# Kernel optimization log

Measured on AMD Instinct MI355X. Metric: run time of the kernel, lower is better.

Reference implementation:

```python
import jax, jax.numpy as jnp
from jax import lax
import numpy as np

B, IMG_H, IMG_W = 8, 256, 512
NUM_CLASSES, P = 20, 32
SCALE, TOPK, IOU_THR = 32.0, 100, 0.5


def conv2d(x, w, b, stride=1, pad=1):
    y = lax.conv_general_dilated(x, w, (stride, stride), [(pad, pad), (pad, pad)],
                                 dimension_numbers=('NCHW', 'OIHW', 'NCHW'))
    return y + b[None, :, None, None]


def bilinear_resize(img, out_h, out_w):
    # img: [..., H, W]; torch F.interpolate(mode='bilinear', align_corners=False)
    H, W = img.shape[-2], img.shape[-1]
    def idx_w(n_in, n_out):
        src = (jnp.arange(n_out, dtype=jnp.float32) + 0.5) * (n_in / n_out) - 0.5
        src = jnp.clip(src, 0.0, n_in - 1)
        i0 = jnp.floor(src).astype(jnp.int32)
        i1 = jnp.minimum(i0 + 1, n_in - 1)
        return i0, i1, src - i0.astype(jnp.float32)
    y0, y1, wy = idx_w(H, out_h)
    x0, x1, wx = idx_w(W, out_w)
    top = img[..., y0, :] * (1.0 - wy)[:, None] + img[..., y1, :] * wy[:, None]
    return top[..., x0] * (1.0 - wx) + top[..., x1] * wx


def generate_anchors(fh, fw):
    ys = (jnp.arange(fh, dtype=jnp.float32) + 0.5) * (IMG_H / fh)
    xs = (jnp.arange(fw, dtype=jnp.float32) + 0.5) * (IMG_W / fw)
    cy, cx = jnp.meshgrid(ys, xs, indexing='ij')
    h = SCALE / 2
    return jnp.stack([cx - h, cy - h, cx + h, cy + h], -1).reshape(-1, 4)


def delta_to_boxes(anchors, deltas):
    a_c = (anchors[:, :2] + anchors[:, 2:]) / 2
    a_wh = anchors[:, 2:] - anchors[:, :2]
    pc = a_c + deltas[..., :2] * a_wh
    pwh = a_wh * jnp.exp(deltas[..., 2:])
    return jnp.concatenate([pc - pwh / 2, pc + pwh / 2], -1)


def nms_single(boxes, scores, labels):
    # torchvision batched_nms: offset boxes per label, greedy NMS, return kept idxs
    N = boxes.shape[0]
    off = labels.astype(boxes.dtype) * (jnp.max(boxes) + 1.0)
    b = boxes + off[:, None]
    order = jnp.argsort(-scores)
    bs = b[order]
    area = (bs[:, 2] - bs[:, 0]) * (bs[:, 3] - bs[:, 1])
    lt = jnp.maximum(bs[:, None, :2], bs[None, :, :2])
    rb = jnp.minimum(bs[:, None, 2:], bs[None, :, 2:])
    wh = jnp.clip(rb - lt, 0.0)
    inter = wh[..., 0] * wh[..., 1]
    iou = inter / (area[:, None] + area[None, :] - inter + 1e-9)
    idxs = jnp.arange(N)
    def body(i, suppressed):
        keep_i = jnp.logical_not(suppressed[i])
        row = (iou[i] > IOU_THR) & (idxs > i)
        return jnp.where(keep_i, suppressed | row, suppressed)
    suppressed = lax.fori_loop(0, N, body, jnp.zeros(N, bool))
    keep_mask = ~suppressed
    rank = jnp.cumsum(keep_mask) - 1
    slots = jnp.where(keep_mask & (rank < TOPK), rank, TOPK)
    out = jnp.full(TOPK + 1, -1, jnp.int32).at[slots].set(order.astype(jnp.int32))
    return out[:TOPK]


def setup_inputs():
    key = jax.random.key(0)
    ks = jax.random.split(key, 17)
    def cw(k, o, i, kh, kw_):
        return jax.random.normal(k, (o, i, kh, kw_), jnp.float32) / np.sqrt(i * kh * kw_)
    return {
        'images': jax.random.normal(ks[0], (B, 3, IMG_H, IMG_W), jnp.float32),
        'w1': cw(ks[1], 64, 3, 3, 3),   'b1': jnp.zeros(64, jnp.float32),
        'w2': cw(ks[2], 128, 64, 3, 3), 'b2': jnp.zeros(128, jnp.float32),
        'w3': cw(ks[3], 256, 128, 3, 3),'b3': jnp.zeros(256, jnp.float32),
        'pw1': cw(ks[4], 256, 256, 3, 3), 'pb1': jnp.zeros(256, jnp.float32),
        'pw2': cw(ks[5], P, 256, 1, 1),   'pb2': jnp.zeros(P, jnp.float32),
        'cw_': cw(ks[6], NUM_CLASSES + 1, 256, 3, 3), 'cb': jnp.zeros(NUM_CLASSES + 1, jnp.float32),
        'bw': cw(ks[7], 4, 256, 3, 3),  'bb': jnp.zeros(4, jnp.float32),
        'kw': cw(ks[8], P, 256, 3, 3),  'kb': jnp.zeros(P, jnp.float32),
    }


def reference(images, w1, b1, w2, b2, w3, b3, pw1, pb1, pw2, pb2, cw_, cb, bw, bb, kw, kb):
    x = jax.nn.relu(conv2d(images, w1, b1, stride=2))
    x = jax.nn.relu(conv2d(x, w2, b2, stride=2))
    feat = jax.nn.relu(conv2d(x, w3, b3, stride=2))          # [B,256,32,64]
    proto = conv2d(jax.nn.relu(conv2d(feat, pw1, pb1)), pw2, pb2, pad=0)  # [B,P,32,64]
    fh, fw = feat.shape[2], feat.shape[3]
    def head(w, b, c):
        return conv2d(feat, w, b).transpose(0, 2, 3, 1).reshape(B, -1, c)
    cls = head(cw_, cb, NUM_CLASSES + 1)     # [B,N,C+1]
    box = head(bw, bb, 4)                    # [B,N,4]
    coef = head(kw, kb, P)                   # [B,N,P]
    anchors = generate_anchors(fh, fw)       # [N,4]
    probs = jax.nn.softmax(cls, -1)[..., :-1]
    scores = probs.max(-1)
    labels = probs.argmax(-1).astype(jnp.int32)
    boxes = delta_to_boxes(anchors, box)     # [B,N,4]
    keep = jax.vmap(nms_single)(boxes, scores, labels)   # [B,100], -1 pad
    valid = keep >= 0
    ki = jnp.clip(keep, 0)
    take = lambda a: jnp.take_along_axis(a, ki[..., None] if a.ndim == 3 else ki, axis=1)
    boxes_k = take(boxes) * valid[..., None]
    scores_k = take(scores) * valid
    labels_k = jnp.where(valid, take(labels), 0)
    coef_k = jnp.take_along_axis(coef, ki[..., None], axis=1)   # [B,100,P]
    m = jax.nn.sigmoid(jnp.einsum('bkp,bphw->bkhw', coef_k, proto))
    masks = bilinear_resize(m, IMG_H, IMG_W) > 0.5
    masks = masks & valid[..., None, None]
    return boxes_k, scores_k, labels_k, masks, valid
```

## Files before the change

kernel.cpp:

```cpp
#include <hip/hip_runtime.h>
#include <hip/hip_bf16.h>
#include <math.h>

#define BB 8
#define NCLS 21
#define NANCH 2048
#define TOPK_N 100

static const size_t OFF_X1HI = 0;
static const size_t OFF_X1LO = 34344960;
static const size_t OFF_X2HI = 68689920;
static const size_t OFF_X2LO = 86261760;
static const size_t OFF_FTHI = 103833600;
static const size_t OFF_FTLO = 113025024;
static const size_t OFF_WT1  = 122216448;
static const size_t OFF_A2H  = 122223616;
static const size_t OFF_A2L  = 122371072;
static const size_t OFF_A3H  = 122518528;
static const size_t OFF_A3L  = 123108352;
static const size_t OFF_AHH  = 123698176;
static const size_t OFF_AHL  = 123993088;
static const size_t OFF_AP1H = 124288000;
static const size_t OFF_AP1L = 125467648;
static const size_t OFF_WTP2 = 126647296;
static const size_t OFF_BH   = 126680064;
static const size_t OFF_HOUT = 126680576;
static const size_t OFF_P1   = 130874880;
static const size_t OFF_PROTO= 147652096;
static const size_t OFF_BOXES= 149749248;
static const size_t OFF_SCORES=150011392;
static const size_t OFF_LABELS=150076928;
static const size_t OFF_ORDER= 150142464;
static const size_t OFF_SB   = 150208000;
static const size_t OFF_IOU  = 150470144;
static const size_t OFF_KEEP = 154664448;
static const size_t OFF_MAXB = 154668032;

static const size_t OUT_BOXES  = 0;
static const size_t OUT_SCORES = 3200;
static const size_t OUT_LABELS = 4000;
static const size_t OUT_MASKS  = 4800;
static const size_t OUT_VALID  = 104862400;

typedef __attribute__((ext_vector_type(8))) short bf16x8;
typedef __attribute__((ext_vector_type(4))) float f32x4;

__device__ __forceinline__ unsigned encf(float f){
  unsigned u = __float_as_uint(f);
  return (u & 0x80000000u) ? ~u : (u | 0x80000000u);
}
__device__ __forceinline__ float decf(unsigned u){
  unsigned b = (u & 0x80000000u) ? (u & 0x7fffffffu) : ~u;
  return __uint_as_float(b);
}
__device__ __forceinline__ short f2bf(float f){
  __hip_bfloat16 h = __float2bfloat16(f);
  return *(short*)&h;
}
__device__ __forceinline__ float bf2f(short h){
  return __uint_as_float(((unsigned)(unsigned short)h) << 16);
}

template<int CIN,int COUT,int KK>
__device__ __forceinline__ void packw_body(int i, const float* __restrict__ w,
                                           float* __restrict__ wT){
  if (i >= CIN*KK*COUT) return;
  int co = i % COUT; int r = i / COUT;
  int ci = r / KK,  k = r % KK;
  wT[i] = w[(co*CIN + ci)*KK + k];
}

template<int CIN,int COUT>
__device__ __forceinline__ void packA_body(int i, const float* __restrict__ w,
                                           short* __restrict__ Ahi, short* __restrict__ Alo){
  constexpr int K = CIN*9;
  constexpr int KS = K/32;
  if (i >= COUT*K) return;
  int sub  = i & 7;
  int lane = (i >> 3) & 63;
  int rest = i >> 9;
  int ks = rest % KS;
  int mt = rest / KS;
  int m = mt*16 + (lane & 15);
  int k = ks*32 + (lane >> 4)*8 + sub;
  int tap = k / CIN, ci = k - tap*CIN;
  float v = w[(m*CIN + ci)*9 + tap];
  short h = f2bf(v);
  Ahi[i] = h;
  Alo[i] = f2bf(v - bf2f(h));
}

__device__ __forceinline__ void packAh_body(int i,
    const float* __restrict__ cw, const float* __restrict__ bw,
    const float* __restrict__ kw, const float* __restrict__ cb,
    const float* __restrict__ bb, const float* __restrict__ kb,
    short* __restrict__ Ahi, short* __restrict__ Alo, float* __restrict__ bh){
  if (i < 64){
    float v = 0.f;
    if (i < 21) v = cb[i]; else if (i < 25) v = bb[i-21]; else if (i < 57) v = kb[i-25];
    bh[i] = v;
  }
  if (i >= 64*2304) return;
  constexpr int KS = 72;
  int sub  = i & 7;
  int lane = (i >> 3) & 63;
  int rest = i >> 9;
  int ks = rest % KS;
  int mt = rest / KS;
  int m = mt*16 + (lane & 15);
  int k = ks*32 + (lane >> 4)*8 + sub;
  int tap = k >> 8, ci = k & 255;
  float v = 0.f;
  if (m < 21)      v = cw[(m*256 + ci)*9 + tap];
  else if (m < 25) v = bw[((m-21)*256 + ci)*9 + tap];
  else if (m < 57) v = kw[((m-25)*256 + ci)*9 + tap];
  short h = f2bf(v);
  Ahi[i] = h;
  Alo[i] = f2bf(v - bf2f(h));
}

__global__ __launch_bounds__(256) void megaprep(
    const float* __restrict__ images, const float* __restrict__ w1, const float* __restrict__ b1,
    const float* __restrict__ w2, short* __restrict__ a2h, short* __restrict__ a2l,
    const float* __restrict__ w3, short* __restrict__ a3h, short* __restrict__ a3l,
    const float* __restrict__ pw1, short* __restrict__ ap1h, short* __restrict__ ap1l,
    const float* __restrict__ cw, const float* __restrict__ bw, const float* __restrict__ kw,
    const float* __restrict__ cb, const float* __restrict__ bb, const float* __restrict__ kb,
    short* __restrict__ ahh, short* __restrict__ ahl, float* __restrict__ bh,
    const float* __restrict__ pw2, float* __restrict__ wTp2,
    short* __restrict__ x1hi, short* __restrict__ x1lo,
    short* __restrict__ x2hi, short* __restrict__ x2lo,
    short* __restrict__ fthi, short* __restrict__ ftlo,
    unsigned* __restrict__ maxb){
  __shared__ float sw[27*64];
  const int blk = blockIdx.x, tid = threadIdx.x;

  if (blk < 583){
    int i = blk*256 + tid;
    if (i < BB) maxb[i] = 0u;
    short *hi, *lo; int Hp, Wp, cell, bg;
    if (i < 49408){
      hi=x1hi; lo=x1lo; Hp=130; Wp=258; cell = i % 772; bg = i / 772;
    } else if (i < 99072){
      int j = i - 49408; hi=x2hi; lo=x2lo; Hp=66; Wp=130; cell = j % 388; bg = j / 388;
    } else if (i < 149248){
      int j = i - 99072; hi=fthi; lo=ftlo; Hp=34; Wp=66; cell = j % 196; bg = j / 196;
    } else return;
    int y, x;
    if (cell < Wp)        { y = 0;      x = cell; }
    else if (cell < 2*Wp) { y = Hp-1;   x = cell - Wp; }
    else { int r = cell - 2*Wp; y = 1 + (r>>1); x = (r&1) ? (Wp-1) : 0; }
    size_t ad = (((size_t)bg*Hp + y)*Wp + x)*8;
    bf16x8 z = (bf16x8){0,0,0,0,0,0,0,0};
    *(bf16x8*)(hi + ad) = z;
    *(bf16x8*)(lo + ad) = z;
    return;
  }
  if (blk < 4935){
    int lb = blk - 583;
    if (lb < 288)        packA_body<64,128>(lb*256+tid, w2, a2h, a2l);
    else if (lb < 1440)  packA_body<128,256>((lb-288)*256+tid, w3, a3h, a3l);
    else if (lb < 3744)  packA_body<256,256>((lb-1440)*256+tid, pw1, ap1h, ap1l);
    else if (lb < 4320)  packAh_body((lb-3744)*256+tid, cw,bw,kw,cb,bb,kb, ahh,ahl,bh);
    else                 packw_body<256,32,1>((lb-4320)*256+tid, pw2, wTp2);
    return;
  }

  const int cblk = blk - 4935;
  const int bxc = cblk & 63;
  const int co0 = ((cblk >> 6) & 3) * 16;
  const int b   = cblk >> 8;
  for (int idx = tid; idx < 1728; idx += 256){
    int r = idx >> 6, co = idx & 63;
    sw[idx] = w1[co*27 + r];
  }
  __syncthreads();

  const int g  = bxc*256 + tid;
  const int y  = g >> 7;
  const int x0 = (g & 127) << 1;

  float acc[16][2];
#pragma unroll
  for (int c=0;c<16;c++){
    float bv = b1[co0+c];
    acc[c][0] = bv; acc[c][1] = bv;
  }
  int   off[3][5];
  float msk[3][5];
#pragma unroll
  for (int kh=0;kh<3;kh++){
    int iy = y*2 - 1 + kh;
    bool okr = (iy >= 0) && (iy < 256);
    int ro = okr ? iy*512 : 0;
#pragma unroll
    for (int t=0;t<5;t++){
      int col = x0*2 - 1 + t;
      bool ok = okr && (col >= 0) && (col < 512);
      off[kh][t] = ok ? (ro + col) : 0;
      msk[kh][t] = ok ? 1.f : 0.f;
    }
  }
  const float* inb = images + (size_t)b*3*256*512;
  for (int ci=0; ci<3; ci++){
    const float* inc = inb + (size_t)ci*256*512;
    float v[3][5];
#pragma unroll
    for (int kh=0;kh<3;kh++)
#pragma unroll
      for (int t=0;t<5;t++)
        v[kh][t] = inc[off[kh][t]] * msk[kh][t];
    const float* wp = sw + ci*9*64 + co0;
#pragma unroll
    for (int kh=0;kh<3;kh++)
#pragma unroll
    for (int kw2=0;kw2<3;kw2++){
      const float* wq = wp + (kh*3+kw2)*64;
#pragma unroll
      for (int c=0;c<16;c++){
        float wv = wq[c];
        acc[c][0] = fmaf(wv, v[kh][2*0+kw2], acc[c][0]);
        acc[c][1] = fmaf(wv, v[kh][2*1+kw2], acc[c][1]);
      }
    }
  }
#pragma unroll
  for (int s=0;s<2;s++){
    short hv[16] __attribute__((aligned(16)));
    short lv[16] __attribute__((aligned(16)));
#pragma unroll
    for (int c=0;c<16;c++){
      float r = fmaxf(acc[c][s], 0.f);
      short h = f2bf(r);
      hv[c] = h;
      lv[c] = f2bf(r - bf2f(h));
    }
#pragma unroll
    for (int g2=0; g2<2; g2++){
      size_t ad = (((size_t)(b*8 + (co0>>3) + g2)*130 + (y+1))*258 + (x0+s+1))*8;
      *(bf16x8*)(x1hi + ad) = *(bf16x8*)(hv + g2*8);
      *(bf16x8*)(x1lo + ad) = *(bf16x8*)(lv + g2*8);
    }
  }
}

template<int CIN,int K,int M,int MW,int NW,int S,int IPH,int IPW,int NXB,
         bool SPLIT,bool STAGELO,bool STAGEREG,int EMODE,int OPH,int OPW>
__device__ __forceinline__ void cgemm_row_body(
    short* sB, int bxi, int byi, int bzi,
    const short* __restrict__ Ahi, const short* __restrict__ Alo,
    const short* __restrict__ Bhi, const short* __restrict__ Blo,
    const float* __restrict__ bias, float* __restrict__ outf,
    short* __restrict__ outhi, short* __restrict__ outlo){
  static_assert(CIN % 32 == 0, "CIN must be multiple of 32");
  constexpr int NT = 64*32;
  constexpr int KS = K/32;
  constexpr int CG = CIN/8;
  constexpr int SW  = 64*S + 2;
  constexpr int SWP = (S==2) ? (SW/2 + 1) : SW;
  constexpr int LOOFF = CG*((S==2)?2:1)*SWP*8;
  constexpr int NTH = NW*64;
  constexpr int NLD = (CG*SW + NTH - 1)/NTH;

  const int b    = bzi;
  const int oy   = bxi / NXB;
  const int xb   = (bxi % NXB) * 64;
  const int wave = threadIdx.x >> 6;
  const int lane = threadIdx.x & 63;
  const int lm = lane & 15, lq = lane >> 4;
  const int m0 = (byi * NW + wave) * (MW*16);
  const int tid = threadIdx.x;

  f32x4 acc[MW][4];
#pragma unroll
  for (int i=0;i<MW;i++)
#pragma unroll
    for (int j=0;j<4;j++) acc[i][j] = (f32x4){0.f,0.f,0.f,0.f};

  const short* Ah_l = Ahi + (size_t)lane*8;
  const short* Al_l = Alo + (size_t)lane*8;
  const int mt0 = m0 >> 4;
  const size_t plane = (size_t)IPH*IPW;
  const short* Bl0 = Blo + ((size_t)b*CG + lq)*plane*8;

  bf16x8 rh[STAGEREG ? NLD : 1];
  bf16x8 rl[(STAGEREG && SPLIT && STAGELO) ? NLD : 1];

  auto LOADS = [&](int iyv){
    const short* srch = Bhi + (((size_t)b*CG*IPH + iyv)*IPW + (size_t)(xb*S))*8;
#pragma unroll
    for (int t=0;t<NLD;t++){
      int c = tid + t*NTH;
      if (c < CG*SW){
        int g = c / SW, p = c - g*SW;
        rh[t] = *(const bf16x8*)(srch + ((size_t)g*plane + p)*8);
      }
    }
    if constexpr (SPLIT && STAGELO){
      const short* srcl = Blo + (((size_t)b*CG*IPH + iyv)*IPW + (size_t)(xb*S))*8;
#pragma unroll
      for (int t=0;t<NLD;t++){
        int c = tid + t*NTH;
        if (c < CG*SW){
          int g = c / SW, p = c - g*SW;
          rl[t] = *(const bf16x8*)(srcl + ((size_t)g*plane + p)*8);
        }
      }
    }
  };
  auto WRITES = [&](){
#pragma unroll
    for (int t=0;t<NLD;t++){
      int c = tid + t*NTH;
      if (c < CG*SW){
        int g = c / SW, p = c - g*SW;
        int dst = (S==2) ? ((g*2 + (p&1))*SWP + (p>>1)) : (g*SW + p);
        *(bf16x8*)(&sB[(size_t)dst*8]) = rh[t];
        if constexpr (SPLIT && STAGELO)
          *(bf16x8*)(&sB[LOOFF + (size_t)dst*8]) = rl[t];
      }
    }
  };

  if constexpr (STAGEREG){
    LOADS(oy*S);
    WRITES();
    __syncthreads();
  }

#pragma unroll 1
  for (int dy=0; dy<3; dy++){
    const int iy = oy*S + dy;
    if constexpr (STAGEREG){
      if (dy < 2) LOADS(oy*S + dy + 1);
    } else {
      __syncthreads();
      {
        const short* srch = Bhi + (((size_t)b*CG*IPH + iy)*IPW + (size_t)(xb*S))*8;
        for (int c = tid; c < CG*SW; c += NTH){
          int g = c / SW, p = c - g*SW;
          int dst = (S==2) ? ((g*2 + (p&1))*SWP + (p>>1)) : (g*SW + p);
          *(bf16x8*)(&sB[(size_t)dst*8]) =
            *(const bf16x8*)(srch + ((size_t)g*plane + p)*8);
        }
        if constexpr (SPLIT && STAGELO){
          const short* srcl = Blo + (((size_t)b*CG*IPH + iy)*IPW + (size_t)(xb*S))*8;
          for (int c = tid; c < CG*SW; c += NTH){
            int g = c / SW, p = c - g*SW;
            int dst = (S==2) ? ((g*2 + (p&1))*SWP + (p>>1)) : (g*SW + p);
            *(bf16x8*)(&sB[LOOFF + (size_t)dst*8]) =
              *(const bf16x8*)(srcl + ((size_t)g*plane + p)*8);
          }
        }
      }
      __syncthreads();
    }
#pragma unroll
    for (int dx=0; dx<3; dx++){
      const int tap = dy*3 + dx;
      const int ksb = tap*(CIN/32);
#pragma unroll
      for (int kc=0; kc<CIN; kc+=32){
        const int ks = ksb + (kc>>5);
        int ra[4];
#pragma unroll
        for (int j=0;j<4;j++){
          int pc = (j*16 + lm)*S + dx;
          ra[j] = (S==2) ? ((((kc>>3) + lq)*2 + (pc&1))*SWP + (pc>>1))
                         : (((kc>>3) + lq)*SW + pc);
        }
        bf16x8 ah[MW], bh_[4];
#pragma unroll
        for (int i=0;i<MW;i++)
          ah[i] = *(const bf16x8*)(Ah_l + ((size_t)(mt0+i)*KS + ks)*512);
#pragma unroll
        for (int j=0;j<4;j++)
          bh_[j] = *(const bf16x8*)(&sB[(size_t)ra[j]*8]);
        if constexpr (SPLIT){
          bf16x8 al[MW], bl_[4];
#pragma unroll
          for (int i=0;i<MW;i++)
            al[i] = *(const bf16x8*)(Al_l + ((size_t)(mt0+i)*KS + ks)*512);
          if constexpr (STAGELO){
#pragma unroll
            for (int j=0;j<4;j++)
              bl_[j] = *(const bf16x8*)(&sB[LOOFF + (size_t)ra[j]*8]);
          } else {
#pragma unroll
            for (int j=0;j<4;j++){
              size_t pix = (size_t)iy*IPW + (size_t)((xb + j*16 + lm)*S + dx);
              bl_[j] = *(const bf16x8*)(Bl0 + ((size_t)(kc>>3)*plane + pix)*8);
            }
          }
#pragma unroll
          for (int j=0;j<4;j++)
#pragma unroll
            for (int i=0;i<MW;i++)
              acc[i][j] = __builtin_amdgcn_mfma_f32_16x16x32_bf16(ah[i], bh_[j], acc[i][j], 0,0,0);
#pragma unroll
          for (int j=0;j<4;j++)
#pragma unroll
            for (int i=0;i<MW;i++)
              acc[i][j] = __builtin_amdgcn_mfma_f32_16x16x32_bf16(ah[i], bl_[j], acc[i][j], 0,0,0);
#pragma unroll
          for (int j=0;j<4;j++)
#pragma unroll
            for (int i=0;i<MW;i++)
              acc[i][j] = __builtin_amdgcn_mfma_f32_16x16x32_bf16(al[i], bh_[j], acc[i][j], 0,0,0);
        } else {
#pragma unroll
          for (int j=0;j<4;j++)
#pragma unroll
            for (int i=0;i<MW;i++)
              acc[i][j] = __builtin_amdgcn_mfma_f32_16x16x32_bf16(ah[i], bh_[j], acc[i][j], 0,0,0);
        }
      }
    }
    if constexpr (STAGEREG){
      if (dy < 2){
        __syncthreads();
        WRITES();
        __syncthreads();
      }
    }
  }

#pragma unroll
  for (int i=0;i<MW;i++){
#pragma unroll
    for (int r=0;r<4;r++){
      const int m = m0 + i*16 + lq*4 + r;
      const float bv = bias[m];
      if constexpr (EMODE == 0){
#pragma unroll
        for (int j=0;j<4;j++){
          const int ox = xb + j*16 + lm;
          float v = fmaxf(acc[i][j][r] + bv, 0.f);
          short h = f2bf(v);
          short l = f2bf(v - bf2f(h));
          size_t ad = ((((size_t)(b*(M/8) + (m>>3))*OPH + (oy+1))*OPW + (ox+1)))*8 + (m&7);
          outhi[ad] = h;
          outlo[ad] = l;
        }
      } else {
        float* cp = outf + ((size_t)b*M + m)*NT + oy*64 + lm;
#pragma unroll
        for (int j=0;j<4;j++){
          float v = acc[i][j][r] + bv;
          if constexpr (EMODE == 2) v = fmaxf(v, 0.f);
          cp[j*16] = v;
        }
      }
    }
  }
}

template<int CIN,int K,int M,int MW,int NW,int S,int IPH,int IPW,int NXB,
         bool SPLIT,bool STAGELO,bool STAGEREG,int EMODE,int OPH,int OPW>
__global__ __launch_bounds__(NW*64) void cgemm_row(
    const short* __restrict__ Ahi, const short* __restrict__ Alo,
    const short* __restrict__ Bhi, const short* __restrict__ Blo,
    const float* __restrict__ bias, float* __restrict__ outf,
    short* __restrict__ outhi, short* __restrict__ outlo){
  constexpr int CG = CIN/8;
  constexpr int SW  = 64*S + 2;
  constexpr int SWP = (S==2) ? (SW/2 + 1) : SW;
  constexpr int LOOFF = CG*((S==2)?2:1)*SWP*8;
  constexpr int BUFS = (SPLIT && STAGELO) ? 2 : 1;
  __shared__ __align__(16) short sB[BUFS*LOOFF];
  cgemm_row_body<CIN,K,M,MW,NW,S,IPH,IPW,NXB,SPLIT,STAGELO,STAGEREG,EMODE,OPH,OPW>(
      sB, blockIdx.x, blockIdx.y, blockIdx.z,
      Ahi, Alo, Bhi, Blo, bias, outf, outhi, outlo);
}

__device__ __forceinline__ void headsdec_body(
    short* sB, int oy, int b,
    const short* __restrict__ Ahi, const short* __restrict__ Alo,
    const short* __restrict__ Bhi, const short* __restrict__ Blo,
    const float* __restrict__ bias, float* __restrict__ hout,
    float* __restrict__ boxes, float* __restrict__ scores,
    int* __restrict__ labels, unsigned* __restrict__ maxb){
  constexpr int KS = 72;
  constexpr int CG = 32;
  constexpr int SW = 66;
  constexpr int IPH = 34, IPW = 66;
  constexpr int LOOFF = CG*SW*8;
  constexpr int NLD = (CG*SW + 255)/256;

  const int wave = threadIdx.x >> 6;
  const int lane = threadIdx.x & 63;
  const int lm = lane & 15, lq = lane >> 4;
  const int tid = threadIdx.x;

  f32x4 acc[4];
#pragma unroll
  for (int j=0;j<4;j++) acc[j] = (f32x4){0.f,0.f,0.f,0.f};

  const short* Ah_l = Ahi + (size_t)lane*8;
  const short* Al_l = Alo + (size_t)lane*8;
  const size_t plane = (size_t)IPH*IPW;

  bf16x8 rh[NLD], rl[NLD];
  auto HLOADS = [&](int iyv){
    const short* srch = Bhi + ((size_t)b*CG*IPH + iyv)*IPW*8;
    const short* srcl = Blo + ((size_t)b*CG*IPH + iyv)*IPW*8;
#pragma unroll
    for (int t=0;t<NLD;t++){
      int c = tid + t*256;
      if (c < CG*SW){
        int g = c / SW, p = c - g*SW;
        rh[t] = *(const bf16x8*)(srch + ((size_t)g*plane + p)*8);
        rl[t] = *(const bf16x8*)(srcl + ((size_t)g*plane + p)*8);
      }
    }
  };
  auto HWRITES = [&](){
#pragma unroll
    for (int t=0;t<NLD;t++){
      int c = tid + t*256;
      if (c < CG*SW){
        *(bf16x8*)(&sB[(size_t)c*8]) = rh[t];
        *(bf16x8*)(&sB[LOOFF + (size_t)c*8]) = rl[t];
      }
    }
  };

  HLOADS(oy);
  HWRITES();
  __syncthreads();

#pragma unroll 1
  for (int dy=0; dy<3; dy++){
    if (dy < 2) HLOADS(oy + dy + 1);
#pragma unroll
    for (int dx=0; dx<3; dx++){
      const int tap = dy*3 + dx;
      const int ksb = tap*8;
#pragma unroll
      for (int kc=0; kc<256; kc+=32){
        const int ks = ksb + (kc>>5);
        int ra[4];
#pragma unroll
        for (int j=0;j<4;j++) ra[j] = ((kc>>3) + lq)*SW + (j*16 + lm) + dx;
        bf16x8 bh_[4], bl_[4];
#pragma unroll
        for (int j=0;j<4;j++){
          bh_[j] = *(const bf16x8*)(&sB[(size_t)ra[j]*8]);
          bl_[j] = *(const bf16x8*)(&sB[LOOFF + (size_t)ra[j]*8]);
        }
        bf16x8 ah = *(const bf16x8*)(Ah_l + ((size_t)wave*KS + ks)*512);
        bf16x8 al = *(const bf16x8*)(Al_l + ((size_t)wave*KS + ks)*512);
#pragma unroll
        for (int j=0;j<4;j++)
          acc[j] = __builtin_amdgcn_mfma_f32_16x16x32_bf16(ah, bh_[j], acc[j], 0,0,0);
#pragma unroll
        for (int j=0;j<4;j++)
          acc[j] = __builtin_amdgcn_mfma_f32_16x16x32_bf16(ah, bl_[j], acc[j], 0,0,0);
#pragma unroll
        for (int j=0;j<4;j++)
          acc[j] = __builtin_amdgcn_mfma_f32_16x16x32_bf16(al, bh_[j], acc[j], 0,0,0);
      }
    }
    if (dy < 2){
      __syncthreads();
      HWRITES();
      __syncthreads();
    }
  }

  __syncthreads();
  float* sF = (float*)sB;
#pragma unroll
  for (int r=0;r<4;r++){
    const int m = wave*16 + lq*4 + r;
    const float bv = bias[m];
    float* cp = hout + ((size_t)b*64 + m)*NANCH + oy*64 + lm;
#pragma unroll
    for (int j=0;j<4;j++){
      float v = acc[j][r] + bv;
      cp[j*16] = v;
      sF[m*68 + j*16 + lm] = v;
    }
  }
  __syncthreads();

  if (tid < 64){
    const int n = oy*64 + tid;
    float l[NCLS];
    float M = -1e30f;
#pragma unroll
    for (int c=0;c<NCLS;c++){ l[c] = sF[c*68 + tid]; M = fmaxf(M, l[c]); }
    float denom = 0.f;
#pragma unroll
    for (int c=0;c<NCLS;c++) denom += expf(l[c]-M);
    float best = -1.f; int bi = 0;
#pragma unroll
    for (int c=0;c<NCLS-1;c++){
      float e = expf(l[c]-M);
      if (e > best){ best = e; bi = c; }
    }
    scores[(size_t)b*NANCH + n] = best/denom;
    labels[(size_t)b*NANCH + n] = bi;

    float dxv = sF[21*68 + tid], dyv = sF[22*68 + tid];
    float dwv = sF[23*68 + tid], dhv = sF[24*68 + tid];
    const int yy = n >> 6, xx = n & 63;
    float cx = (xx+0.5f)*8.f, cy = (yy+0.5f)*8.f;
    float px = cx + dxv*32.f, py = cy + dyv*32.f;
    float pw = 32.f*expf(dwv), ph = 32.f*expf(dhv);
    float x1 = px - 0.5f*pw, y1 = py - 0.5f*ph;
    float x2 = px + 0.5f*pw, y2 = py + 0.5f*ph;
    float* bo = boxes + ((size_t)b*NANCH + n)*4;
    bo[0]=x1; bo[1]=y1; bo[2]=x2; bo[3]=y2;
    float mx = fmaxf(fmaxf(x1,y1), fmaxf(x2,y2));
#pragma unroll
    for (int off=32; off>0; off>>=1) mx = fmaxf(mx, __shfl_down(mx, off));
    if (tid == 0) atomicMax(maxb + b, encf(mx));
  }
}

__global__ __launch_bounds__(256) void headpw1k(
    const short* __restrict__ ahh, const short* __restrict__ ahl,
    const short* __restrict__ ap1h,
    const short* __restrict__ fthi, const short* __restrict__ ftlo,
    const float* __restrict__ bh, const float* __restrict__ pb1,
    float* __restrict__ hout, float* __restrict__ p1,
    float* __restrict__ boxes, float* __restrict__ scores,
    int* __restrict__ labels, unsigned* __restrict__ maxb){
  __shared__ __align__(16) short smem[33792];
  const int bx = blockIdx.x, b = blockIdx.z;
  if (bx < 32){
    headsdec_body(smem, bx, b, ahh, ahl, fthi, ftlo, bh, hout,
                  boxes, scores, labels, maxb);
  } else {
    const int lx = bx - 32;
    cgemm_row_body<256,2304,256,2,4,1,34,66,1,false,false,true,2,1,1>(
        smem, lx & 31, lx >> 5, b, ap1h, ap1h, fthi, fthi, pb1, p1, nullptr, nullptr);
  }
}

__global__ void __launch_bounds__(1024) pw2sortk(
    const float* __restrict__ p1, const float* __restrict__ wT,
    const float* __restrict__ biasp, float* __restrict__ proto,
    const float* __restrict__ scores, const float* __restrict__ boxes,
    const int* __restrict__ labels, const unsigned* __restrict__ maxb,
    int* __restrict__ order, float* __restrict__ sb){
  __shared__ float sc[NANCH];
  __shared__ int   id[NANCH];
  const int bx = blockIdx.x, t = threadIdx.x;
  if (bx < 16){
    const int b  = bx >> 1;
    const int sp = (bx & 1)*1024 + t;
    float acc[32];
#pragma unroll
    for (int c=0;c<32;c++) acc[c] = biasp[c];
    const float* pb = p1 + (size_t)b*256*NANCH + sp;
    for (int ci=0;ci<256;ci++){
      float v = pb[(size_t)ci*NANCH];
      const float* wq = wT + ci*32;
#pragma unroll
      for (int c=0;c<32;c++) acc[c] = fmaf(v, wq[c], acc[c]);
    }
#pragma unroll
    for (int c=0;c<32;c++)
      proto[((size_t)b*32 + c)*NANCH + sp] = acc[c];
    return;
  }
  const int b = bx - 16;
  for (int i=t;i<NANCH;i+=1024){ sc[i]=scores[(size_t)b*NANCH+i]; id[i]=i; }
  __syncthreads();
  for (int k=2;k<=NANCH;k<<=1){
    for (int j=k>>1;j>0;j>>=1){
      for (int i=t;i<NANCH;i+=1024){
        int ixj = i ^ j;
        if (ixj > i){
          float sa=sc[i], sb_=sc[ixj]; int ia=id[i], ib=id[ixj];
          bool dir = ((i & k) == 0);
          bool before_ba = (sb_ > sa) || (sb_ == sa && ib < ia);
          if (before_ba == dir){ sc[i]=sb_; sc[ixj]=sa; id[i]=ib; id[ixj]=ia; }
        }
      }
      __syncthreads();
    }
  }
  float mboff = decf(maxb[b]) + 1.0f;
  for (int r=t;r<NANCH;r+=1024){
    int o = id[r];
    order[(size_t)b*NANCH + r] = o;
    float off = (float)labels[(size_t)b*NANCH + o] * mboff;
    const float* bo = boxes + ((size_t)b*NANCH + o)*4;
    float* sp = sb + ((size_t)b*NANCH + r)*4;
    sp[0]=bo[0]+off; sp[1]=bo[1]+off; sp[2]=bo[2]+off; sp[3]=bo[3]+off;
  }
}

__global__ void ioumask(const float* __restrict__ sb, unsigned long long* __restrict__ iou){
  const int b = blockIdx.y;
  const int gid = blockIdx.x*blockDim.x + threadIdx.x;
  const int i = gid >> 5, w = gid & 31;
  const float* base = sb + (size_t)b*NANCH*4;
  unsigned long long bits = 0ull;
  const int j0 = w << 6;
  if (j0 + 63 > i){
    float x1=base[i*4], y1=base[i*4+1], x2=base[i*4+2], y2=base[i*4+3];
    float ai = (x2-x1)*(y2-y1);
    for (int jj=0;jj<64;jj++){
      int j = j0 + jj;
      if (j > i){
        float bx1=base[j*4], by1=base[j*4+1], bx2=base[j*4+2], by2=base[j*4+3];
        float lx=fmaxf(x1,bx1), ly=fmaxf(y1,by1);
        float rx=fminf(x2,bx2), ry=fminf(y2,by2);
        float ww=fmaxf(rx-lx,0.f), hh=fmaxf(ry-ly,0.f);
        float inter = ww*hh;
        float aj = (bx2-bx1)*(by2-by1);
        float v = inter/(ai + aj - inter + 1e-9f);
        if (v > 0.5f) bits |= (1ull << jj);
      }
    }
  }
  iou[((size_t)b*NANCH + i)*32 + w] = bits;
}

__global__ void nmsgather(const unsigned long long* __restrict__ iou,
                          const int* __restrict__ order,
                          const float* __restrict__ boxes, const float* __restrict__ scores,
                          const int* __restrict__ labels,
                          int* __restrict__ keep, float* __restrict__ out){
  const int b = blockIdx.x, lane = threadIdx.x;
  __shared__ int s_keep[TOPK_N];
  unsigned long long sup = 0ull;
  int k = 0, i = 0;
  while (k < TOPK_N){
    unsigned long long avail = (lane < 32) ? ~sup : 0ull;
    const int wi = i >> 6;
    if (lane < wi) avail = 0ull;
    else if (lane == wi) avail &= (~0ull) << (i & 63);
    unsigned long long ball = __ballot(avail != 0ull);
    if (!ball) break;
    int w0 = (int)__builtin_ctzll(ball);
    unsigned long long aw = __shfl(avail, w0);
    int b0 = (int)__builtin_ctzll(aw);
    i = (w0 << 6) + b0;
    int ov = order[(size_t)b*NANCH + i];
    if (lane == 0) s_keep[k] = ov;
    k++;
    unsigned long long row = (lane < 32) ? iou[((size_t)b*NANCH + i)*32 + lane] : 0ull;
    sup |= row;
    i++;
    if (i >= NANCH) break;
  }
  __syncthreads();
  for (int r = lane; r < TOPK_N; r += 64){
    int kv = (r < k) ? s_keep[r] : -1;
    keep[b*TOPK_N + r] = kv;
    float valid = (kv >= 0) ? 1.f : 0.f;
    int kc = (kv < 0) ? 0 : kv;
    const float* bo = boxes + ((size_t)b*NANCH + kc)*4;
#pragma unroll
    for (int c=0;c<4;c++) out[OUT_BOXES + ((size_t)b*TOPK_N + r)*4 + c] = bo[c]*valid;
    out[OUT_SCORES + b*TOPK_N + r] = scores[(size_t)b*NANCH + kc]*valid;
    out[OUT_LABELS + b*TOPK_N + r] = (kv >= 0) ? (float)labels[(size_t)b*NANCH + kc] : 0.f;
    out[OUT_VALID  + b*TOPK_N + r] = valid;
  }
}

__global__ __launch_bounds__(256) void maskresize(const int* __restrict__ keep,
    const float* __restrict__ hout, const float* __restrict__ proto,
    float* __restrict__ out){
  const int b = blockIdx.y, r = blockIdx.x;
  float* obase = out + OUT_MASKS + ((size_t)b*TOPK_N + r)*131072;
  int ki = keep[b*TOPK_N + r];
  if (ki < 0){
    float4 z = make_float4(0.f,0.f,0.f,0.f);
    for (int idx = threadIdx.x; idx < 32768; idx += 256)
      ((float4*)obase)[idx] = z;
    return;
  }
  __shared__ float cf[32];
  __shared__ float sm[NANCH];
  if (threadIdx.x < 32)
    cf[threadIdx.x] = hout[((size_t)b*64 + 25 + threadIdx.x)*NANCH + ki];
  __syncthreads();
  for (int s = threadIdx.x; s < NANCH; s += 256){
    float acc = 0.f;
#pragma unroll
    for (int p=0;p<32;p++) acc = fmaf(cf[p], proto[((size_t)b*32 + p)*NANCH + s], acc);
    sm[s] = 1.f/(1.f + expf(-acc));
  }
  __syncthreads();
  for (int pid = threadIdx.x; pid < 32768; pid += 256){
    const int y  = pid >> 7;
    const int x4 = (pid & 127) << 2;
    float sy = (y + 0.5f)*0.125f - 0.5f;
    sy = fminf(fmaxf(sy, 0.f), 31.f);
    int y0 = (int)floorf(sy);
    int y1 = min(y0+1, 31);
    float wy = sy - (float)y0;
    const float* r0 = sm + y0*64;
    const float* r1 = sm + y1*64;
    float res[4];
#pragma unroll
    for (int kk=0;kk<4;kk++){
      int x = x4 + kk;
      float sx = (x + 0.5f)*0.125f - 0.5f;
      sx = fminf(fmaxf(sx, 0.f), 63.f);
      int x0 = (int)floorf(sx);
      int x1 = min(x0+1, 63);
      float wx = sx - (float)x0;
      float t0 = r0[x0]*(1.f-wy) + r1[x0]*wy;
      float t1 = r0[x1]*(1.f-wy) + r1[x1]*wy;
      float v  = t0*(1.f-wx) + t1*wx;
      res[kk] = (v > 0.5f) ? 1.f : 0.f;
    }
    *(float4*)(obase + y*512 + x4) = make_float4(res[0], res[1], res[2], res[3]);
  }
}

extern "C" void kernel_launch(void* const* d_in, const int* in_sizes, int n_in,
                              void* d_out, int out_size, void* d_ws, size_t ws_size,
                              hipStream_t stream) {
  const float* images=(const float*)d_in[0];
  const float* w1=(const float*)d_in[1];  const float* b1=(const float*)d_in[2];
  const float* w2=(const float*)d_in[3];  const float* b2=(const float*)d_in[4];
  const float* w3=(const float*)d_in[5];  const float* b3=(const float*)d_in[6];
  const float* pw1=(const float*)d_in[7]; const float* pb1=(const float*)d_in[8];
  const float* pw2=(const float*)d_in[9]; const float* pb2=(const float*)d_in[10];
  const float* cw=(const float*)d_in[11]; const float* cb=(const float*)d_in[12];
  const float* bw=(const float*)d_in[13]; const float* bb=(const float*)d_in[14];
  const float* kw=(const float*)d_in[15]; const float* kb=(const float*)d_in[16];
  float* out = (float*)d_out;
  char* ws = (char*)d_ws;

  short* x1hi = (short*)(ws + OFF_X1HI);
  short* x1lo = (short*)(ws + OFF_X1LO);
  short* x2hi = (short*)(ws + OFF_X2HI);
  short* x2lo = (short*)(ws + OFF_X2LO);
  short* fthi = (short*)(ws + OFF_FTHI);
  short* ftlo = (short*)(ws + OFF_FTLO);
  short* a2h  = (short*)(ws + OFF_A2H);
  short* a2l  = (short*)(ws + OFF_A2L);
  short* a3h  = (short*)(ws + OFF_A3H);
  short* a3l  = (short*)(ws + OFF_A3L);
  short* ahh  = (short*)(ws + OFF_AHH);
  short* ahl  = (short*)(ws + OFF_AHL);
  short* ap1h = (short*)(ws + OFF_AP1H);
  short* ap1l = (short*)(ws + OFF_AP1L);
  float* wTp2 = (float*)(ws + OFF_WTP2);
  float* bh   = (float*)(ws + OFF_BH);
  float* hout = (float*)(ws + OFF_HOUT);
  float* p1   = (float*)(ws + OFF_P1);
  float* proto= (float*)(ws + OFF_PROTO);
  float* boxes= (float*)(ws + OFF_BOXES);
  float* scores=(float*)(ws + OFF_SCORES);
  int*   labels=(int*)  (ws + OFF_LABELS);
  int*   order =(int*)  (ws + OFF_ORDER);
  float* sb   = (float*)(ws + OFF_SB);
  unsigned long long* iou = (unsigned long long*)(ws + OFF_IOU);
  int*   keep = (int*)  (ws + OFF_KEEP);
  unsigned* maxb = (unsigned*)(ws + OFF_MAXB);

  megaprep<<<dim3(6983), 256, 0, stream>>>(
      images, w1, b1, w2, a2h, a2l, w3, a3h, a3l, pw1, ap1h, ap1l,
      cw, bw, kw, cb, bb, kb, ahh, ahl, bh, pw2, wTp2,
      x1hi, x1lo, x2hi, x2lo, fthi, ftlo, maxb);

  cgemm_row<64,576,128,2,4,2,130,258,2,true,true,true,0,66,130>
      <<<dim3(128,1,BB), 256, 0, stream>>>(a2h, a2l, x1hi, x1lo, b2, nullptr, x2hi, x2lo);

  cgemm_row<128,1152,256,2,4,2,66,130,1,true,true,true,0,34,66>
      <<<dim3(32,2,BB), 256, 0, stream>>>(a3h, a3l, x2hi, x2lo, b3, nullptr, fthi, ftlo);

  headpw1k<<<dim3(96,1,BB), 256, 0, stream>>>(ahh, ahl, ap1h, fthi, ftlo,
                                              bh, pb1, hout, p1,
                                              boxes, scores, labels, maxb);

  pw2sortk<<<dim3(24), 1024, 0, stream>>>(p1, wTp2, pb2, proto,
                                          scores, boxes, labels, maxb, order, sb);

  ioumask<<<dim3(256,BB), 256, 0, stream>>>(sb, iou);
  nmsgather<<<dim3(BB), 64, 0, stream>>>(iou, order, boxes, scores, labels, keep, out);

  maskresize<<<dim3(TOPK_N,BB), 256, 0, stream>>>(keep, hout, proto, out);
}
```

Baseline: 889.4 us.

## Fuse IoU mask and greedy NMS into sort kernel using shared-memory lazy IoU

Replaces the separate ioumask and nmsgather kernels, and the global order/sb buffers, with a greedy NMS loop inside the sort kernel. Each kept box's IoU against all later boxes is computed on the fly from shared memory by 1024 threads, and the suppression bitmask is updated through wave ballots. This drops two launches and the full 2048x2048 IoU bitmask write and read, at the cost of up to 100 serialized block-wide iterations, each with barriers. The maskresize grid is also flattened to 1D with batch as the fastest index.

```diff
diff --git a/kernel.cpp b/kernel.cpp
--- a/kernel.cpp
+++ b/kernel.cpp
@@ -13,7 +13,6 @@
 static const size_t OFF_X2LO = 86261760;
 static const size_t OFF_FTHI = 103833600;
 static const size_t OFF_FTLO = 113025024;
-static const size_t OFF_WT1  = 122216448;
 static const size_t OFF_A2H  = 122223616;
 static const size_t OFF_A2L  = 122371072;
 static const size_t OFF_A3H  = 122518528;
@@ -30,9 +29,6 @@
 static const size_t OFF_BOXES= 149749248;
 static const size_t OFF_SCORES=150011392;
 static const size_t OFF_LABELS=150076928;
-static const size_t OFF_ORDER= 150142464;
-static const size_t OFF_SB   = 150208000;
-static const size_t OFF_IOU  = 150470144;
 static const size_t OFF_KEEP = 154664448;
 static const size_t OFF_MAXB = 154668032;
 
@@ -639,14 +635,18 @@
   }
 }
 
-__global__ void __launch_bounds__(1024) pw2sortk(
+__global__ void __launch_bounds__(1024) pw2nms(
     const float* __restrict__ p1, const float* __restrict__ wT,
     const float* __restrict__ biasp, float* __restrict__ proto,
     const float* __restrict__ scores, const float* __restrict__ boxes,
     const int* __restrict__ labels, const unsigned* __restrict__ maxb,
-    int* __restrict__ order, float* __restrict__ sb){
+    int* __restrict__ keep, float* __restrict__ out){
   __shared__ float sc[NANCH];
   __shared__ int   id[NANCH];
+  __shared__ float sbL[NANCH*4];
+  __shared__ unsigned long long sup[32];
+  __shared__ int s_keep[TOPK_N];
+  __shared__ int s_next;
   const int bx = blockIdx.x, t = threadIdx.x;
   if (bx < 16){
     const int b  = bx >> 1;
@@ -668,6 +668,7 @@
   }
   const int b = bx - 16;
   for (int i=t;i<NANCH;i+=1024){ sc[i]=scores[(size_t)b*NANCH+i]; id[i]=i; }
+  if (t < 32) sup[t] = 0ull;
   __syncthreads();
   for (int k=2;k<=NANCH;k<<=1){
     for (int j=k>>1;j>0;j>>=1){
@@ -686,71 +687,71 @@
   float mboff = decf(maxb[b]) + 1.0f;
   for (int r=t;r<NANCH;r+=1024){
     int o = id[r];
-    order[(size_t)b*NANCH + r] = o;
     float off = (float)labels[(size_t)b*NANCH + o] * mboff;
     const float* bo = boxes + ((size_t)b*NANCH + o)*4;
-    float* sp = sb + ((size_t)b*NANCH + r)*4;
-    sp[0]=bo[0]+off; sp[1]=bo[1]+off; sp[2]=bo[2]+off; sp[3]=bo[3]+off;
-  }
-}
-
-__global__ void ioumask(const float* __restrict__ sb, unsigned long long* __restrict__ iou){
-  const int b = blockIdx.y;
-  const int gid = blockIdx.x*blockDim.x + threadIdx.x;
-  const int i = gid >> 5, w = gid & 31;
-  const float* base = sb + (size_t)b*NANCH*4;
-  unsigned long long bits = 0ull;
-  const int j0 = w << 6;
-  if (j0 + 63 > i){
-    float x1=base[i*4], y1=base[i*4+1], x2=base[i*4+2], y2=base[i*4+3];
+    sbL[r*4]   = bo[0]+off; sbL[r*4+1] = bo[1]+off;
+    sbL[r*4+2] = bo[2]+off; sbL[r*4+3] = bo[3]+off;
+  }
+  __syncthreads();
+  int k = 0, i = 0;
+  while (true){
+    if (k >= TOPK_N) break;
+    if (t < 64){
+      unsigned long long avail = (t < 32) ? ~sup[t] : 0ull;
+      const int wi = i >> 6;
+      if ((int)t < wi) avail = 0ull;
+      else if ((int)t == wi) avail &= (~0ull) << (i & 63);
+      unsigned long long ball = __ballot(avail != 0ull);
+      int nxt = -1;
+      if (ball){
+        int w0 = (int)__builtin_ctzll(ball);
+        unsigned long long aw = __shfl(avail, w0);
+        int b0 = (int)__builtin_ctzll(aw);
+        nxt = (w0 << 6) + b0;
+      }
+      if (t == 0) s_next = nxt;
+    }
+    __syncthreads();
+    i = s_next;
+    if (i < 0) break;
+    if (t == 0) s_keep[k] = id[i];
+    k++;
+    float x1 = sbL[i*4], y1 = sbL[i*4+1], x2 = sbL[i*4+2], y2 = sbL[i*4+3];
     float ai = (x2-x1)*(y2-y1);
-    for (int jj=0;jj<64;jj++){
-      int j = j0 + jj;
+    bool f0 = false, f1 = false;
+    {
+      int j = t;
       if (j > i){
-        float bx1=base[j*4], by1=base[j*4+1], bx2=base[j*4+2], by2=base[j*4+3];
+        float bx1=sbL[j*4], by1=sbL[j*4+1], bx2=sbL[j*4+2], by2=sbL[j*4+3];
         float lx=fmaxf(x1,bx1), ly=fmaxf(y1,by1);
         float rx=fminf(x2,bx2), ry=fminf(y2,by2);
         float ww=fmaxf(rx-lx,0.f), hh=fmaxf(ry-ly,0.f);
         float inter = ww*hh;
         float aj = (bx2-bx1)*(by2-by1);
-        float v = inter/(ai + aj - inter + 1e-9f);
-        if (v > 0.5f) bits |= (1ull << jj);
-      }
-    }
-  }
-  iou[((size_t)b*NANCH + i)*32 + w] = bits;
-}
-
-__global__ void nmsgather(const unsigned long long* __restrict__ iou,
-                          const int* __restrict__ order,
-                          const float* __restrict__ boxes, const float* __restrict__ scores,
-                          const int* __restrict__ labels,
-                          int* __restrict__ keep, float* __restrict__ out){
-  const int b = blockIdx.x, lane = threadIdx.x;
-  __shared__ int s_keep[TOPK_N];
-  unsigned long long sup = 0ull;
-  int k = 0, i = 0;
-  while (k < TOPK_N){
-    unsigned long long avail = (lane < 32) ? ~sup : 0ull;
-    const int wi = i >> 6;
-    if (lane < wi) avail = 0ull;
-    else if (lane == wi) avail &= (~0ull) << (i & 63);
-    unsigned long long ball = __ballot(avail != 0ull);
-    if (!ball) break;
-    int w0 = (int)__builtin_ctzll(ball);
-    unsigned long long aw = __shfl(avail, w0);
-    int b0 = (int)__builtin_ctzll(aw);
-    i = (w0 << 6) + b0;
-    int ov = order[(size_t)b*NANCH + i];
-    if (lane == 0) s_keep[k] = ov;
-    k++;
-    unsigned long long row = (lane < 32) ? iou[((size_t)b*NANCH + i)*32 + lane] : 0ull;
-    sup |= row;
+        f0 = (inter/(ai + aj - inter + 1e-9f)) > 0.5f;
+      }
+      j = t + 1024;
+      if (j > i){
+        float bx1=sbL[j*4], by1=sbL[j*4+1], bx2=sbL[j*4+2], by2=sbL[j*4+3];
+        float lx=fmaxf(x1,bx1), ly=fmaxf(y1,by1);
+        float rx=fminf(x2,bx2), ry=fminf(y2,by2);
+        float ww=fmaxf(rx-lx,0.f), hh=fmaxf(ry-ly,0.f);
+        float inter = ww*hh;
+        float aj = (bx2-bx1)*(by2-by1);
+        f1 = (inter/(ai + aj - inter + 1e-9f)) > 0.5f;
+      }
+    }
+    unsigned long long b0m = __ballot(f0);
+    unsigned long long b1m = __ballot(f1);
+    if ((t & 63) == 0){
+      sup[t >> 6]        |= b0m;
+      sup[16 + (t >> 6)] |= b1m;
+    }
     i++;
-    if (i >= NANCH) break;
+    __syncthreads();
   }
   __syncthreads();
-  for (int r = lane; r < TOPK_N; r += 64){
+  for (int r = t; r < TOPK_N; r += 1024){
     int kv = (r < k) ? s_keep[r] : -1;
     keep[b*TOPK_N + r] = kv;
     float valid = (kv >= 0) ? 1.f : 0.f;
@@ -767,7 +768,7 @@
 __global__ __launch_bounds__(256) void maskresize(const int* __restrict__ keep,
     const float* __restrict__ hout, const float* __restrict__ proto,
     float* __restrict__ out){
-  const int b = blockIdx.y, r = blockIdx.x;
+  const int b = blockIdx.x & 7, r = blockIdx.x >> 3;
   float* obase = out + OUT_MASKS + ((size_t)b*TOPK_N + r)*131072;
   int ki = keep[b*TOPK_N + r];
   if (ki < 0){
@@ -853,9 +854,6 @@
   float* boxes= (float*)(ws + OFF_BOXES);
   float* scores=(float*)(ws + OFF_SCORES);
   int*   labels=(int*)  (ws + OFF_LABELS);
-  int*   order =(int*)  (ws + OFF_ORDER);
-  float* sb   = (float*)(ws + OFF_SB);
-  unsigned long long* iou = (unsigned long long*)(ws + OFF_IOU);
   int*   keep = (int*)  (ws + OFF_KEEP);
   unsigned* maxb = (unsigned*)(ws + OFF_MAXB);
 
@@ -874,11 +872,8 @@
                                               bh, pb1, hout, p1,
                                               boxes, scores, labels, maxb);
 
-  pw2sortk<<<dim3(24), 1024, 0, stream>>>(p1, wTp2, pb2, proto,
-                                          scores, boxes, labels, maxb, order, sb);
-
-  ioumask<<<dim3(256,BB), 256, 0, stream>>>(sb, iou);
-  nmsgather<<<dim3(BB), 64, 0, stream>>>(iou, order, boxes, scores, labels, keep, out);
-
-  maskresize<<<dim3(TOPK_N,BB), 256, 0, stream>>>(keep, hout, proto, out);
-}
+  pw2nms<<<dim3(24), 1024, 0, stream>>>(p1, wTp2, pb2, proto,
+                                        scores, boxes, labels, maxb, keep, out);
+
+  maskresize<<<dim3(800), 256, 0, stream>>>(keep, hout, proto, out);
+}
```

Measured after the change: 836.1 us (median of 2 runs). 6.0% less time.
